# Optimization experiments

Measured on AMD Instinct MI355X. Metric: run time of the kernel, lower is better.

Reference implementation:

```python
import jax, jax.numpy as jnp
import numpy as np

# ---- MACE hyperparameters (match init_kwargs) ----
R_MAX = 5.0      # radial cutoff
P_CUT = 6        # polynomial cutoff exponent
NUM_BESSEL = 8
C = 32           # hidden channels
N_NODES = 50000
N_EDGES = 800000
N_SPECIES = 10
N_GRAPHS = 32
AVG_NEIGH = 16.0
RADIAL_HIDDEN = 64
N_LM = 9                      # (lmax+1)^2, lmax=2
L_OF_LM = np.array([0, 1, 1, 1, 2, 2, 2, 2, 2])


def _sph_harm_l2(v):
    """Real spherical harmonics up to l=2, e3nn 'component' normalization.
    v: [E,3] unit vectors -> [E,9]."""
    x, y, z = v[:, 0], v[:, 1], v[:, 2]
    s3, s5, s15 = 3.0 ** 0.5, 5.0 ** 0.5, 15.0 ** 0.5
    return jnp.stack([
        jnp.ones_like(x),                 # l=0
        s3 * x, s3 * y, s3 * z,           # l=1
        s15 * x * y, s15 * y * z,         # l=2
        (s5 / 2.0) * (3.0 * z * z - 1.0),
        s15 * x * z,
        (s15 / 2.0) * (x * x - y * y),
    ], axis=-1)


def _radial_basis(r):
    """Bessel basis * polynomial cutoff. r: [E] -> [E, NUM_BESSEL]."""
    n = jnp.arange(1, NUM_BESSEL + 1, dtype=r.dtype)
    safe_r = jnp.maximum(r, 1e-9)
    bessel = jnp.sqrt(2.0 / R_MAX) * jnp.sin(n * jnp.pi * safe_r[:, None] / R_MAX) / safe_r[:, None]
    u = r / R_MAX
    p = float(P_CUT)
    fcut = (1.0 - ((p + 1.0) * (p + 2.0) / 2.0) * u ** P_CUT
            + p * (p + 2.0) * u ** (P_CUT + 1)
            - (p * (p + 1.0) / 2.0) * u ** (P_CUT + 2))
    fcut = jnp.where(u < 1.0, fcut, 0.0)
    return bessel * fcut[:, None]


def setup_inputs() -> dict:
    key = jax.random.key(0)
    ks = jax.random.split(key, 12)
    positions = 1.5 * jax.random.normal(ks[0], (N_NODES, 3), dtype=jnp.float32)
    shifts = jnp.zeros((N_EDGES, 3), dtype=jnp.float32)
    species = jax.random.randint(ks[1], (N_NODES,), 0, N_SPECIES)
    node_attrs = jax.nn.one_hot(species, N_SPECIES, dtype=jnp.float32)
    edge_index = jax.random.randint(ks[2], (2, N_EDGES), 0, N_NODES)
    batch = jnp.sort(jax.random.randint(ks[3], (N_NODES,), 0, N_GRAPHS))
    # learned parameters
    W_embed = jax.random.normal(ks[4], (N_SPECIES, C), jnp.float32) / np.sqrt(N_SPECIES)
    rW1 = jax.random.normal(ks[5], (NUM_BESSEL, RADIAL_HIDDEN), jnp.float32) / np.sqrt(NUM_BESSEL)
    rb1 = jnp.zeros((RADIAL_HIDDEN,), jnp.float32)
    rW2 = jax.random.normal(ks[6], (RADIAL_HIDDEN, RADIAL_HIDDEN), jnp.float32) / np.sqrt(RADIAL_HIDDEN)
    rb2 = jnp.zeros((RADIAL_HIDDEN,), jnp.float32)
    rW3 = jax.random.normal(ks[7], (RADIAL_HIDDEN, C * 3), jnp.float32) / np.sqrt(RADIAL_HIDDEN)
    W_mix = jax.random.normal(ks[8], (3, C, C), jnp.float32) / np.sqrt(C)   # per-l channel mixing
    w_quad = jax.random.normal(ks[9], (3,), jnp.float32) * 0.1              # correlation-2 invariant weights
    W_readout = jax.random.normal(ks[10], (C,), jnp.float32) / np.sqrt(C)
    atomic_energies = jax.random.normal(ks[11], (N_SPECIES,), jnp.float32)
    return {"node_attrs": node_attrs, "positions": positions, "shifts": shifts,
            "W_embed": W_embed, "rW1": rW1, "rb1": rb1, "rW2": rW2, "rb2": rb2,
            "rW3": rW3, "W_mix": W_mix, "w_quad": w_quad, "W_readout": W_readout,
            "atomic_energies": atomic_energies, "edge_index": edge_index, "batch": batch}


def reference(node_attrs, positions, shifts, W_embed, rW1, rb1, rW2, rb2, rW3,
              W_mix, w_quad, W_readout, atomic_energies, edge_index, batch):
    sender, receiver = edge_index[0], edge_index[1]
    # edge vectors / lengths (get_edge_vectors_and_lengths)
    vec = positions[receiver] - positions[sender] + shifts          # [E,3]
    length = jnp.linalg.norm(vec, axis=-1)                          # [E]
    unit = vec / jnp.maximum(length, 1e-9)[:, None]
    # radial embedding (Bessel * polynomial cutoff) -> MLP -> per-(channel,l) weights
    rb = _radial_basis(length)                                      # [E,8]
    h1 = jax.nn.silu(rb @ rW1 + rb1)
    h2 = jax.nn.silu(h1 @ rW2 + rb2)
    R = (h2 @ rW3).reshape(-1, C, 3)                                # [E,C,3]
    Y = _sph_harm_l2(unit)                                          # [E,9]
    # node embedding (LinearNodeEmbeddingBlock)
    h = node_attrs @ W_embed                                        # [N,C]
    # channelwise CG tensor product message (scalar source x Y_l -> l) + scatter-sum
    l_of_lm = jnp.asarray(L_OF_LM)
    msg = R[:, :, l_of_lm] * h[sender][:, :, None] * Y[:, None, :]  # [E,C,9]
    A = jax.ops.segment_sum(msg, receiver, num_segments=N_NODES) / AVG_NEIGH  # [N,C,9]
    # per-l linear channel mixing (o3.Linear)
    W_lm = W_mix[l_of_lm]                                           # [9,C,C]
    A2 = jnp.einsum('mcd,ncm->ndm', W_lm, A)                        # [N,C,9]
    # symmetric contraction (correlation 2): rotation-invariant features
    sq = A2 * A2                                                    # [N,C,9]
    onehot_l = jax.nn.one_hot(l_of_lm, 3, dtype=A2.dtype)           # [9,3]
    l_norms = jnp.einsum('ncm,ml->ncl', sq, onehot_l)               # [N,C,3]
    B = A2[:, :, 0] + l_norms @ w_quad                              # [N,C]
    # readout + atomic reference energies, pooled per graph
    node_e = B @ W_readout + node_attrs @ atomic_energies           # [N]
    graph_e = jax.ops.segment_sum(node_e, batch, num_segments=N_GRAPHS)
    return graph_e
```

## Files before the change

### kernel.cpp

```cpp
#include <hip/hip_runtime.h>
#include <hip/hip_bf16.h>

#define NNODES 50000
#define NEDGES 800000
#define NGRAPHS 32
#define NSPEC 10
#define CC 32
#define RH 64
#define NB 8

#define EBLK 128
#define NCHUNK (NEDGES / EBLK)
#define GSTR 136
#define YSTRF 132
#define ASTR 72
#define RBSTR 40
#define SCAN_N 53248

typedef __bf16 bf16x8 __attribute__((ext_vector_type(8)));
typedef float f32x4 __attribute__((ext_vector_type(4)));

__device__ __forceinline__ unsigned pack2bf(float a, float b) {
    return (unsigned)__bfloat16_as_ushort(__float2bfloat16(a)) |
           ((unsigned)__bfloat16_as_ushort(__float2bfloat16(b)) << 16);
}

__global__ __launch_bounds__(256) void prep_hist_kernel(
    const float* __restrict__ attrs, const int* __restrict__ eidx,
    const float* __restrict__ rW1, const float* __restrict__ rb1,
    const float* __restrict__ rW2, const float* __restrict__ rW3,
    int* __restrict__ counts, int* __restrict__ rank, int* __restrict__ species,
    __hip_bfloat16* __restrict__ W1T, __hip_bfloat16* __restrict__ W2T,
    __hip_bfloat16* __restrict__ W3T) {
    int g = blockIdx.x * 256 + threadIdx.x;
    if (g < NEDGES) rank[g] = atomicAdd(&counts[eidx[NEDGES + g]], 1);
    if (g < NNODES) {
        float acc = 0.f;
#pragma unroll
        for (int s = 0; s < NSPEC; ++s) acc += attrs[g * NSPEC + s] * (float)s;
        species[g] = (int)(acc + 0.5f);
    }
    if (g < 64 * 32) {
        int c = g >> 5, k = g & 31;
        float v = (k < 8) ? rW1[k * 64 + c] : ((k == 8) ? rb1[c] : 0.f);
        W1T[g] = __float2bfloat16(v);
    }
    if (g < 64 * 64) {
        int c = g >> 6, k = g & 63;
        W2T[g] = __float2bfloat16(rW2[k * 64 + c]);
    }
    if (g < 96 * 64) {
        int c = g >> 6, k = g & 63;
        W3T[g] = __float2bfloat16(rW3[k * 96 + c]);
    }
}

__global__ __launch_bounds__(1024) void scan_kernel(const int* __restrict__ counts,
                                                    int* __restrict__ offsets) {
    __shared__ int sums[1024];
    const int t = threadIdx.x;
    const int base = t * 52;
    int loc[52];
    int s = 0;
#pragma unroll
    for (int i = 0; i < 13; ++i) {
        int4 v = *(const int4*)&counts[base + i * 4];
        loc[i * 4 + 0] = v.x; loc[i * 4 + 1] = v.y;
        loc[i * 4 + 2] = v.z; loc[i * 4 + 3] = v.w;
        s += v.x + v.y + v.z + v.w;
    }
    sums[t] = s;
    __syncthreads();
    for (int off = 1; off < 1024; off <<= 1) {
        int add = (t >= off) ? sums[t - off] : 0;
        __syncthreads();
        sums[t] += add;
        __syncthreads();
    }
    int run = sums[t] - s;
#pragma unroll
    for (int i = 0; i < 13; ++i) {
        int4 o;
        o.x = run; run += loc[i * 4 + 0];
        o.y = run; run += loc[i * 4 + 1];
        o.z = run; run += loc[i * 4 + 2];
        o.w = run; run += loc[i * 4 + 3];
        *(int4*)&offsets[base + i * 4] = o;
    }
}

__global__ __launch_bounds__(256) void scatter_kernel(const int* __restrict__ eidx,
                                                      const int* __restrict__ offsets,
                                                      const int* __restrict__ rank,
                                                      int* __restrict__ perm) {
    int e = blockIdx.x * 256 + threadIdx.x;
    if (e >= NEDGES) return;
    int rcv = eidx[NEDGES + e];
    perm[offsets[rcv] + rank[e]] = e;
}

__device__ __forceinline__ void flushseg(float* __restrict__ A, int node, int cur,
                                         int nseg, int cbase, int j, float aj, float a8) {
    float* Ap = A + (size_t)node * (CC * 9) + cbase * 9;
    if (cur == 0 || cur == nseg - 1) {
        atomicAdd(Ap + j, aj);
        if (j == 0) atomicAdd(Ap + 8, a8);
    } else {
        Ap[j] = aj;
        if (j == 0) Ap[8] = a8;
    }
}

template <int P>
__device__ __forceinline__ void pass_store_reduce(
    const f32x4 (&acc3)[4][6], const int (&sp_r)[4][4],
    __hip_bfloat16* Gt, const float* Yt, const float* WembLds,
    const unsigned short* rcv_s, const unsigned long long* bal_s,
    float* __restrict__ A, int tid, int w, int lnlo, int q4) {
#pragma unroll
    for (int nti = 0; nti < 3; ++nti) {
        const int nt = P * 3 + nti;
        const int col = nt * 16 + lnlo;
        const int cch = col / 3;
        const int s = nti * 16 + lnlo;
#pragma unroll
        for (int mt = 0; mt < 4; ++mt) {
            const float f0 = acc3[mt][nt][0] * WembLds[sp_r[mt][0] * 32 + cch];
            const float f1 = acc3[mt][nt][1] * WembLds[sp_r[mt][1] * 32 + cch];
            const float f2 = acc3[mt][nt][2] * WembLds[sp_r[mt][2] * 32 + cch];
            const float f3 = acc3[mt][nt][3] * WembLds[sp_r[mt][3] * 32 + cch];
            uint2 pk;
            pk.x = pack2bf(f0, f1);
            pk.y = pack2bf(f2, f3);
            *(uint2*)&Gt[s * GSTR + w * 64 + mt * 16 + q4 * 4] = pk;
        }
    }
    __syncthreads();

    {
        const int c = tid >> 3;
        const int j = tid & 7;
        const int l_j = (j == 0) ? 0 : ((j < 4) ? 1 : 2);
        const uint4* gj = (const uint4*)(Gt + (3 * c + l_j) * GSTR);
        const uint4* g8 = (const uint4*)(Gt + (3 * c + 2) * GSTR);
        const float4* yj = (const float4*)(Yt + j * YSTRF);
        const float4* y8f = (const float4*)(Yt + 8 * YSTRF);
        const unsigned long long b0 = bal_s[0], b1 = bal_s[1];
        const int nseg = __popcll(b0) + __popcll(b1);
        const int cbase = P * 16 + c;

        float aj = 0.f, a8 = 0.f;
        int cur = 0;
        int node = rcv_s[0];

        for (int ch = 0; ch < 16; ++ch) {
            unsigned msk = (unsigned)(((ch < 8) ? (b0 >> (ch * 8)) : (b1 >> ((ch - 8) * 8))) & 0xffull);
            if (ch == 0) msk &= ~1u;
            const uint4 gv = gj[ch];
            const float4 ya = yj[2 * ch];
            const float4 yb = yj[2 * ch + 1];
            uint4 gv8 = {0, 0, 0, 0};
            float4 y8a = {0.f, 0.f, 0.f, 0.f}, y8b = {0.f, 0.f, 0.f, 0.f};
            if (j == 0) { gv8 = g8[ch]; y8a = y8f[2 * ch]; y8b = y8f[2 * ch + 1]; }
            const unsigned gw[4] = {gv.x, gv.y, gv.z, gv.w};
            const unsigned gw8[4] = {gv8.x, gv8.y, gv8.z, gv8.w};
            const float yf[8] = {ya.x, ya.y, ya.z, ya.w, yb.x, yb.y, yb.z, yb.w};
            const float yf8[8] = {y8a.x, y8a.y, y8a.z, y8a.w, y8b.x, y8b.y, y8b.z, y8b.w};
#pragma unroll
            for (int i = 0; i < 8; ++i) {
                if (msk & (1u << i)) {
                    flushseg(A, node, cur, nseg, cbase, j, aj, a8);
                    aj = 0.f; a8 = 0.f; ++cur;
                    node = rcv_s[ch * 8 + i];
                }
                const unsigned gu = gw[i >> 1];
                const float gf = __uint_as_float((i & 1) ? (gu & 0xffff0000u) : (gu << 16));
                aj = fmaf(gf, yf[i], aj);
                if (j == 0) {
                    const unsigned hu = gw8[i >> 1];
                    const float hf = __uint_as_float((i & 1) ? (hu & 0xffff0000u) : (hu << 16));
                    a8 = fmaf(hf, yf8[i], a8);
                }
            }
        }
        flushseg(A, node, cur, nseg, cbase, j, aj, a8);
    }
    __syncthreads();
}

__global__ __launch_bounds__(EBLK, 3) void edge_kernel(
    const float* __restrict__ pos, const float* __restrict__ shifts,
    const int* __restrict__ eidx, const int* __restrict__ perm,
    const __hip_bfloat16* __restrict__ W1T, const __hip_bfloat16* __restrict__ W2T,
    const __hip_bfloat16* __restrict__ W3T, const float* __restrict__ rb2,
    const int* __restrict__ species, const float* __restrict__ Wemb,
    float* __restrict__ A) {
    __shared__ __align__(16) short smem_u[128 * ASTR];
    __shared__ __align__(16) float Yt[9 * YSTRF];
    __shared__ float WembLds[NSPEC * CC];
    __shared__ float rb2L[RH];
    __shared__ unsigned short rcv_s[EBLK];
    __shared__ unsigned char spec_s[EBLK];
    __shared__ unsigned long long bal_s[2];

    __hip_bfloat16* act = (__hip_bfloat16*)smem_u;
    __hip_bfloat16* Gt = (__hip_bfloat16*)smem_u;
    __hip_bfloat16* rbA = (__hip_bfloat16*)smem_u;

    const int tid = threadIdx.x;
    const int lane = tid & 63;
    const int w = tid >> 6;
    const int lnlo = lane & 15;
    const int q4 = lane >> 4;

    const int slot = blockIdx.x * EBLK + tid;
    const int eid = perm[slot];
    const int snd = eidx[eid];
    const int rcv = eidx[NEDGES + eid];

    const float vx = pos[rcv * 3 + 0] - pos[snd * 3 + 0] + shifts[eid * 3 + 0];
    const float vy = pos[rcv * 3 + 1] - pos[snd * 3 + 1] + shifts[eid * 3 + 1];
    const float vz = pos[rcv * 3 + 2] - pos[snd * 3 + 2] + shifts[eid * 3 + 2];
    const float r = sqrtf(vx * vx + vy * vy + vz * vz);
    const float safe_r = fmaxf(r, 1e-9f);
    const float rinv = 1.f / safe_r;
    const float ux = vx * rinv, uy = vy * rinv, uz = vz * rinv;

    {
        const float s3 = 1.7320508075688772f;
        const float s15 = 3.872983346207417f;
        const float s15h = 1.9364916731037085f;
        const float s5h = 1.118033988749895f;
        Yt[0 * YSTRF + tid] = 1.f;
        Yt[1 * YSTRF + tid] = s3 * ux;
        Yt[2 * YSTRF + tid] = s3 * uy;
        Yt[3 * YSTRF + tid] = s3 * uz;
        Yt[4 * YSTRF + tid] = s15 * ux * uy;
        Yt[5 * YSTRF + tid] = s15 * uy * uz;
        Yt[6 * YSTRF + tid] = s5h * (3.f * uz * uz - 1.f);
        Yt[7 * YSTRF + tid] = s15 * ux * uz;
        Yt[8 * YSTRF + tid] = s15h * (ux * ux - uy * uy);
        rcv_s[tid] = (unsigned short)rcv;
        spec_s[tid] = (unsigned char)species[snd];
        for (int i = tid; i < NSPEC * CC; i += EBLK) WembLds[i] = Wemb[i];
        if (tid < RH) rb2L[tid] = rb2[tid];
    }

    {
        const float u = r * 0.2f;
        const float u2 = u * u;
        const float u6 = u2 * u2 * u2;
        const float u7 = u6 * u;
        const float u8v = u7 * u;
        float fcut = 1.f - 28.f * u6 + 48.f * u7 - 21.f * u8v;
        fcut = (u < 1.f) ? fcut : 0.f;
        const float pref = 0.632455532f * rinv * fcut;
        float rb[NB];
#pragma unroll
        for (int k = 0; k < NB; ++k) {
            const float fk = (float)(k + 1) * 0.628318530718f;
            rb[k] = __sinf(fk * safe_r) * pref;
        }
        uint4 v0, v1;
        v0.x = pack2bf(rb[0], rb[1]); v0.y = pack2bf(rb[2], rb[3]);
        v0.z = pack2bf(rb[4], rb[5]); v0.w = pack2bf(rb[6], rb[7]);
        v1.x = 0x3F80u; v1.y = 0u; v1.z = 0u; v1.w = 0u;
        uint4 vz4 = {0u, 0u, 0u, 0u};
        *(uint4*)&rbA[tid * RBSTR + 0] = v0;
        *(uint4*)&rbA[tid * RBSTR + 8] = v1;
        *(uint4*)&rbA[tid * RBSTR + 16] = vz4;
        *(uint4*)&rbA[tid * RBSTR + 24] = vz4;
    }

    __syncthreads();
    {
        const bool head = (tid == 0) || (rcv_s[tid] != rcv_s[tid - 1]);
        const unsigned long long bal = __ballot(head);
        if ((tid & 63) == 0) bal_s[tid >> 6] = bal;
    }

    f32x4 acc1[4][4];
#pragma unroll
    for (int mt = 0; mt < 4; ++mt)
#pragma unroll
        for (int nt = 0; nt < 4; ++nt) acc1[mt][nt] = (f32x4){0.f, 0.f, 0.f, 0.f};
    {
        bf16x8 a1[4], b1[4];
#pragma unroll
        for (int mt = 0; mt < 4; ++mt)
            a1[mt] = *(const bf16x8*)&rbA[(w * 64 + mt * 16 + lnlo) * RBSTR + q4 * 8];
#pragma unroll
        for (int nt = 0; nt < 4; ++nt)
            b1[nt] = *(const bf16x8*)&W1T[(nt * 16 + lnlo) * 32 + q4 * 8];
        __syncthreads();
#pragma unroll
        for (int mt = 0; mt < 4; ++mt)
#pragma unroll
            for (int nt = 0; nt < 4; ++nt)
                acc1[mt][nt] = __builtin_amdgcn_mfma_f32_16x16x32_bf16(
                    a1[mt], b1[nt], acc1[mt][nt], 0, 0, 0);
    }

#pragma unroll
    for (int mt = 0; mt < 4; ++mt)
#pragma unroll
        for (int nt = 0; nt < 4; ++nt)
#pragma unroll
            for (int rr = 0; rr < 4; ++rr) {
                const float x = acc1[mt][nt][rr];
                act[(w * 64 + mt * 16 + q4 * 4 + rr) * ASTR + nt * 16 + lnlo] =
                    __float2bfloat16(x / (1.f + __expf(-x)));
            }
    __syncthreads();

    f32x4 acc2[4][4];
#pragma unroll
    for (int mt = 0; mt < 4; ++mt)
#pragma unroll
        for (int nt = 0; nt < 4; ++nt) acc2[mt][nt] = (f32x4){0.f, 0.f, 0.f, 0.f};
    {
        bf16x8 a2[4][2], b2[4][2];
#pragma unroll
        for (int mt = 0; mt < 4; ++mt)
#pragma unroll
            for (int kk = 0; kk < 2; ++kk)
                a2[mt][kk] = *(const bf16x8*)&act[(w * 64 + mt * 16 + lnlo) * ASTR + kk * 32 + q4 * 8];
#pragma unroll
        for (int nt = 0; nt < 4; ++nt)
#pragma unroll
            for (int kk = 0; kk < 2; ++kk)
                b2[nt][kk] = *(const bf16x8*)&W2T[(nt * 16 + lnlo) * 64 + kk * 32 + q4 * 8];
#pragma unroll
        for (int kk = 0; kk < 2; ++kk)
#pragma unroll
            for (int mt = 0; mt < 4; ++mt)
#pragma unroll
                for (int nt = 0; nt < 4; ++nt)
                    acc2[mt][nt] = __builtin_amdgcn_mfma_f32_16x16x32_bf16(
                        a2[mt][kk], b2[nt][kk], acc2[mt][nt], 0, 0, 0);
    }
    __syncthreads();

#pragma unroll
    for (int mt = 0; mt < 4; ++mt)
#pragma unroll
        for (int nt = 0; nt < 4; ++nt) {
            const float bias = rb2L[nt * 16 + lnlo];
#pragma unroll
            for (int rr = 0; rr < 4; ++rr) {
                const float x = acc2[mt][nt][rr] + bias;
                act[(w * 64 + mt * 16 + q4 * 4 + rr) * ASTR + nt * 16 + lnlo] =
                    __float2bfloat16(x / (1.f + __expf(-x)));
            }
        }
    __syncthreads();

    f32x4 acc3[4][6];
#pragma unroll
    for (int mt = 0; mt < 4; ++mt)
#pragma unroll
        for (int nt = 0; nt < 6; ++nt) acc3[mt][nt] = (f32x4){0.f, 0.f, 0.f, 0.f};
    {
        bf16x8 a3[4][2], b3[6][2];
#pragma unroll
        for (int mt = 0; mt < 4; ++mt)
#pragma unroll
            for (int kk = 0; kk < 2; ++kk)
                a3[mt][kk] = *(const bf16x8*)&act[(w * 64 + mt * 16 + lnlo) * ASTR + kk * 32 + q4 * 8];
#pragma unroll
        for (int nt = 0; nt < 6; ++nt)
#pragma unroll
            for (int kk = 0; kk < 2; ++kk)
                b3[nt][kk] = *(const bf16x8*)&W3T[(nt * 16 + lnlo) * 64 + kk * 32 + q4 * 8];
#pragma unroll
        for (int kk = 0; kk < 2; ++kk)
#pragma unroll
            for (int mt = 0; mt < 4; ++mt)
#pragma unroll
                for (int nt = 0; nt < 6; ++nt)
                    acc3[mt][nt] = __builtin_amdgcn_mfma_f32_16x16x32_bf16(
                        a3[mt][kk], b3[nt][kk], acc3[mt][nt], 0, 0, 0);
    }
    __syncthreads();

    int sp_r[4][4];
#pragma unroll
    for (int mt = 0; mt < 4; ++mt)
#pragma unroll
        for (int rr = 0; rr < 4; ++rr)
            sp_r[mt][rr] = (int)spec_s[w * 64 + mt * 16 + q4 * 4 + rr];

    pass_store_reduce<0>(acc3, sp_r, Gt, Yt, WembLds, rcv_s, bal_s, A, tid, w, lnlo, q4);
    pass_store_reduce<1>(acc3, sp_r, Gt, Yt, WembLds, rcv_s, bal_s, A, tid, w, lnlo, q4);
}

__global__ __launch_bounds__(256) void node_kernel(
    const float* __restrict__ A, const float* __restrict__ Wmix,
    const float* __restrict__ wquad, const float* __restrict__ Wread,
    const float* __restrict__ attrs, const float* __restrict__ ae,
    const int* __restrict__ batch, float* __restrict__ out) {
    __shared__ float Ald[8][CC * 9];
    __shared__ float ne_s[8];
    __shared__ int g_s[8];
    const int t = threadIdx.x;
    const int ln = t >> 5;
    const int d = t & 31;
    const int n = blockIdx.x * 8 + ln;

    const float* Arow = A + (size_t)n * (CC * 9);
#pragma unroll
    for (int i = 0; i < 9; ++i) Ald[ln][d + 32 * i] = Arow[d + 32 * i] * (1.f / 16.f);
    __syncthreads();

    float A2[9];
#pragma unroll
    for (int m = 0; m < 9; ++m) {
        const int l = (m == 0) ? 0 : ((m < 4) ? 1 : 2);
        float acc = 0.f;
#pragma unroll
        for (int cch = 0; cch < CC; ++cch)
            acc = fmaf(Wmix[(l * CC + cch) * CC + d], Ald[ln][cch * 9 + m], acc);
        A2[m] = acc;
    }

    const float q0 = wquad[0], q1 = wquad[1], q2 = wquad[2];
    const float n0 = A2[0] * A2[0];
    const float n1 = A2[1] * A2[1] + A2[2] * A2[2] + A2[3] * A2[3];
    const float n2 = A2[4] * A2[4] + A2[5] * A2[5] + A2[6] * A2[6] + A2[7] * A2[7] + A2[8] * A2[8];
    const float B = A2[0] + n0 * q0 + n1 * q1 + n2 * q2;

    float v = B * Wread[d];
#pragma unroll
    for (int off = 16; off; off >>= 1) v += __shfl_xor(v, off, 32);

    if (d == 0) {
        float ne = v;
#pragma unroll
        for (int s = 0; s < NSPEC; ++s) ne += attrs[n * NSPEC + s] * ae[s];
        ne_s[ln] = ne;
        g_s[ln] = batch[n];
    }
    __syncthreads();
    if (t == 0) {
        float acc = ne_s[0];
        int g = g_s[0];
#pragma unroll
        for (int i = 1; i < 8; ++i) {
            if (g_s[i] == g) acc += ne_s[i];
            else { atomicAdd(&out[g], acc); g = g_s[i]; acc = ne_s[i]; }
        }
        atomicAdd(&out[g], acc);
    }
}

extern "C" void kernel_launch(void* const* d_in, const int* in_sizes, int n_in,
                              void* d_out, int out_size, void* d_ws, size_t ws_size,
                              hipStream_t stream) {
    const float* attrs  = (const float*)d_in[0];
    const float* pos    = (const float*)d_in[1];
    const float* shifts = (const float*)d_in[2];
    const float* Wemb   = (const float*)d_in[3];
    const float* rW1    = (const float*)d_in[4];
    const float* rb1    = (const float*)d_in[5];
    const float* rW2    = (const float*)d_in[6];
    const float* rb2    = (const float*)d_in[7];
    const float* rW3    = (const float*)d_in[8];
    const float* Wmix   = (const float*)d_in[9];
    const float* wquad  = (const float*)d_in[10];
    const float* Wread  = (const float*)d_in[11];
    const float* ae     = (const float*)d_in[12];
    const int* eidx     = (const int*)d_in[13];
    const int* batch    = (const int*)d_in[14];
    float* out = (float*)d_out;

    char* wsp = (char*)d_ws;
    float* A      = (float*)wsp;  wsp += (size_t)NNODES * CC * 9 * 4;
    int* rank     = (int*)A;
    int* perm     = (int*)wsp;    wsp += (size_t)NEDGES * 4;
    int* offsets  = (int*)wsp;    wsp += (size_t)SCAN_N * 4;
    int* counts   = (int*)wsp;    wsp += (size_t)SCAN_N * 4;
    int* species  = (int*)wsp;    wsp += (size_t)NNODES * 4;
    __hip_bfloat16* W1T = (__hip_bfloat16*)wsp; wsp += 64 * 32 * 2;
    __hip_bfloat16* W2T = (__hip_bfloat16*)wsp; wsp += 64 * 64 * 2;
    __hip_bfloat16* W3T = (__hip_bfloat16*)wsp; wsp += 96 * 64 * 2;

    hipMemsetAsync(counts, 0, (size_t)SCAN_N * sizeof(int), stream);
    hipMemsetAsync(out, 0, NGRAPHS * sizeof(float), stream);

    prep_hist_kernel<<<NEDGES / 256, 256, 0, stream>>>(attrs, eidx, rW1, rb1, rW2, rW3,
                                                       counts, rank, species, W1T, W2T, W3T);
    scan_kernel<<<1, 1024, 0, stream>>>(counts, offsets);
    scatter_kernel<<<NEDGES / 256, 256, 0, stream>>>(eidx, offsets, rank, perm);

    hipMemsetAsync(A, 0, (size_t)NNODES * CC * 9 * sizeof(float), stream);

    edge_kernel<<<NCHUNK, EBLK, 0, stream>>>(pos, shifts, eidx, perm,
                                             W1T, W2T, W3T, rb2, species, Wemb, A);
    node_kernel<<<NNODES / 8, 256, 0, stream>>>(A, Wmix, wquad, Wread, attrs, ae, batch, out);
}
```

Baseline: 321.1 us.

## Replace full A memset with boundary-only zeroing and transpose radial MLP MFMAs

Drops the full memset of the node accumulator A. A small kernel now zeroes only the rows of receivers at chunk boundaries, which are the only rows that get atomic adds. Interior segments are written directly, and node_kernel masks nodes with zero in-degree using counts, so stale workspace data is ignored. The radial MLP MFMAs are also transposed so that silu outputs can be stored as packed 8-byte writes. The l=2 m=8 reduction moves to lane j=7 to reuse its own G row, and species extraction reads attrs through shared memory with coalesced loads. This relies on every row being fully written or zeroed. Interior writes overlap the A buffer that also holds rank, which is safe only because of the launch ordering.

```diff
diff --git a/kernel.cpp b/kernel.cpp
--- a/kernel.cpp
+++ b/kernel.cpp
@@ -24,6 +24,7 @@
     return (unsigned)__bfloat16_as_ushort(__float2bfloat16(a)) |
            ((unsigned)__bfloat16_as_ushort(__float2bfloat16(b)) << 16);
 }
+__device__ __forceinline__ float silu(float x) { return x / (1.f + __expf(-x)); }
 
 __global__ __launch_bounds__(256) void prep_hist_kernel(
     const float* __restrict__ attrs, const int* __restrict__ eidx,
@@ -32,13 +33,23 @@
     int* __restrict__ counts, int* __restrict__ rank, int* __restrict__ species,
     __hip_bfloat16* __restrict__ W1T, __hip_bfloat16* __restrict__ W2T,
     __hip_bfloat16* __restrict__ W3T) {
-    int g = blockIdx.x * 256 + threadIdx.x;
+    __shared__ float at[256 * NSPEC];
+    const int tid = threadIdx.x;
+    int g = blockIdx.x * 256 + tid;
     if (g < NEDGES) rank[g] = atomicAdd(&counts[eidx[NEDGES + g]], 1);
-    if (g < NNODES) {
-        float acc = 0.f;
-#pragma unroll
-        for (int s = 0; s < NSPEC; ++s) acc += attrs[g * NSPEC + s] * (float)s;
-        species[g] = (int)(acc + 0.5f);
+    const int nbase = blockIdx.x * 256;
+    if (nbase < NNODES) {
+        for (int i = tid; i < 256 * NSPEC; i += 256) {
+            int idx = nbase * NSPEC + i;
+            at[i] = (idx < NNODES * NSPEC) ? attrs[idx] : 0.f;
+        }
+        __syncthreads();
+        if (g < NNODES) {
+            float acc = 0.f;
+#pragma unroll
+            for (int s = 0; s < NSPEC; ++s) acc += at[tid * NSPEC + s] * (float)s;
+            species[g] = (int)(acc + 0.5f);
+        }
     }
     if (g < 64 * 32) {
         int c = g >> 5, k = g & 31;
@@ -99,15 +110,27 @@
     perm[offsets[rcv] + rank[e]] = e;
 }
 
+__global__ __launch_bounds__(576) void zero_bounds_kernel(const int* __restrict__ perm,
+                                                          const int* __restrict__ eidx,
+                                                          float* __restrict__ A) {
+    const int c = blockIdx.x;
+    const int t = threadIdx.x;
+    const int slot = (t < 288) ? c * EBLK : (c * EBLK + EBLK - 1);
+    const int e = perm[slot];
+    const int rcv = eidx[NEDGES + e];
+    A[(size_t)rcv * (CC * 9) + (t % 288)] = 0.f;
+}
+
 __device__ __forceinline__ void flushseg(float* __restrict__ A, int node, int cur,
-                                         int nseg, int cbase, int j, float aj, float a8) {
+                                         int nseg, int cbase, int j, bool wr8,
+                                         float aj, float a8) {
     float* Ap = A + (size_t)node * (CC * 9) + cbase * 9;
     if (cur == 0 || cur == nseg - 1) {
         atomicAdd(Ap + j, aj);
-        if (j == 0) atomicAdd(Ap + 8, a8);
+        if (wr8) atomicAdd(Ap + 8, a8);
     } else {
         Ap[j] = aj;
-        if (j == 0) Ap[8] = a8;
+        if (wr8) Ap[8] = a8;
     }
 }
 
@@ -140,9 +163,9 @@
     {
         const int c = tid >> 3;
         const int j = tid & 7;
+        const bool m8 = (j == 7);
         const int l_j = (j == 0) ? 0 : ((j < 4) ? 1 : 2);
         const uint4* gj = (const uint4*)(Gt + (3 * c + l_j) * GSTR);
-        const uint4* g8 = (const uint4*)(Gt + (3 * c + 2) * GSTR);
         const float4* yj = (const float4*)(Yt + j * YSTRF);
         const float4* y8f = (const float4*)(Yt + 8 * YSTRF);
         const unsigned long long b0 = bal_s[0], b1 = bal_s[1];
@@ -159,31 +182,25 @@
             const uint4 gv = gj[ch];
             const float4 ya = yj[2 * ch];
             const float4 yb = yj[2 * ch + 1];
-            uint4 gv8 = {0, 0, 0, 0};
             float4 y8a = {0.f, 0.f, 0.f, 0.f}, y8b = {0.f, 0.f, 0.f, 0.f};
-            if (j == 0) { gv8 = g8[ch]; y8a = y8f[2 * ch]; y8b = y8f[2 * ch + 1]; }
+            if (m8) { y8a = y8f[2 * ch]; y8b = y8f[2 * ch + 1]; }
             const unsigned gw[4] = {gv.x, gv.y, gv.z, gv.w};
-            const unsigned gw8[4] = {gv8.x, gv8.y, gv8.z, gv8.w};
             const float yf[8] = {ya.x, ya.y, ya.z, ya.w, yb.x, yb.y, yb.z, yb.w};
             const float yf8[8] = {y8a.x, y8a.y, y8a.z, y8a.w, y8b.x, y8b.y, y8b.z, y8b.w};
 #pragma unroll
             for (int i = 0; i < 8; ++i) {
                 if (msk & (1u << i)) {
-                    flushseg(A, node, cur, nseg, cbase, j, aj, a8);
+                    flushseg(A, node, cur, nseg, cbase, j, m8, aj, a8);
                     aj = 0.f; a8 = 0.f; ++cur;
                     node = rcv_s[ch * 8 + i];
                 }
                 const unsigned gu = gw[i >> 1];
                 const float gf = __uint_as_float((i & 1) ? (gu & 0xffff0000u) : (gu << 16));
                 aj = fmaf(gf, yf[i], aj);
-                if (j == 0) {
-                    const unsigned hu = gw8[i >> 1];
-                    const float hf = __uint_as_float((i & 1) ? (hu & 0xffff0000u) : (hu << 16));
-                    a8 = fmaf(hf, yf8[i], a8);
-                }
+                if (m8) a8 = fmaf(gf, yf8[i], a8);
             }
         }
-        flushseg(A, node, cur, nseg, cbase, j, aj, a8);
+        flushseg(A, node, cur, nseg, cbase, j, m8, aj, a8);
     }
     __syncthreads();
 }
@@ -281,78 +298,81 @@
 
     f32x4 acc1[4][4];
 #pragma unroll
-    for (int mt = 0; mt < 4; ++mt)
-#pragma unroll
-        for (int nt = 0; nt < 4; ++nt) acc1[mt][nt] = (f32x4){0.f, 0.f, 0.f, 0.f};
-    {
-        bf16x8 a1[4], b1[4];
-#pragma unroll
-        for (int mt = 0; mt < 4; ++mt)
-            a1[mt] = *(const bf16x8*)&rbA[(w * 64 + mt * 16 + lnlo) * RBSTR + q4 * 8];
-#pragma unroll
-        for (int nt = 0; nt < 4; ++nt)
-            b1[nt] = *(const bf16x8*)&W1T[(nt * 16 + lnlo) * 32 + q4 * 8];
+    for (int jt = 0; jt < 4; ++jt)
+#pragma unroll
+        for (int et = 0; et < 4; ++et) acc1[jt][et] = (f32x4){0.f, 0.f, 0.f, 0.f};
+    {
+        bf16x8 wf[4], af[4];
+#pragma unroll
+        for (int jt = 0; jt < 4; ++jt)
+            wf[jt] = *(const bf16x8*)&W1T[(jt * 16 + lnlo) * 32 + q4 * 8];
+#pragma unroll
+        for (int et = 0; et < 4; ++et)
+            af[et] = *(const bf16x8*)&rbA[(w * 64 + et * 16 + lnlo) * RBSTR + q4 * 8];
         __syncthreads();
 #pragma unroll
-        for (int mt = 0; mt < 4; ++mt)
-#pragma unroll
-            for (int nt = 0; nt < 4; ++nt)
-                acc1[mt][nt] = __builtin_amdgcn_mfma_f32_16x16x32_bf16(
-                    a1[mt], b1[nt], acc1[mt][nt], 0, 0, 0);
-    }
-
-#pragma unroll
-    for (int mt = 0; mt < 4; ++mt)
-#pragma unroll
-        for (int nt = 0; nt < 4; ++nt)
-#pragma unroll
-            for (int rr = 0; rr < 4; ++rr) {
-                const float x = acc1[mt][nt][rr];
-                act[(w * 64 + mt * 16 + q4 * 4 + rr) * ASTR + nt * 16 + lnlo] =
-                    __float2bfloat16(x / (1.f + __expf(-x)));
-            }
+        for (int jt = 0; jt < 4; ++jt)
+#pragma unroll
+            for (int et = 0; et < 4; ++et)
+                acc1[jt][et] = __builtin_amdgcn_mfma_f32_16x16x32_bf16(
+                    wf[jt], af[et], acc1[jt][et], 0, 0, 0);
+    }
+
+#pragma unroll
+    for (int jt = 0; jt < 4; ++jt) {
+        const int ch0 = jt * 16 + q4 * 4;
+#pragma unroll
+        for (int et = 0; et < 4; ++et) {
+            const int e = w * 64 + et * 16 + lnlo;
+            uint2 pk;
+            pk.x = pack2bf(silu(acc1[jt][et][0]), silu(acc1[jt][et][1]));
+            pk.y = pack2bf(silu(acc1[jt][et][2]), silu(acc1[jt][et][3]));
+            *(uint2*)&act[e * ASTR + ch0] = pk;
+        }
+    }
     __syncthreads();
 
     f32x4 acc2[4][4];
 #pragma unroll
-    for (int mt = 0; mt < 4; ++mt)
-#pragma unroll
-        for (int nt = 0; nt < 4; ++nt) acc2[mt][nt] = (f32x4){0.f, 0.f, 0.f, 0.f};
-    {
-        bf16x8 a2[4][2], b2[4][2];
-#pragma unroll
-        for (int mt = 0; mt < 4; ++mt)
+    for (int jt = 0; jt < 4; ++jt)
+#pragma unroll
+        for (int et = 0; et < 4; ++et) acc2[jt][et] = (f32x4){0.f, 0.f, 0.f, 0.f};
+    {
+        bf16x8 wf[4][2], af[4][2];
+#pragma unroll
+        for (int jt = 0; jt < 4; ++jt)
 #pragma unroll
             for (int kk = 0; kk < 2; ++kk)
-                a2[mt][kk] = *(const bf16x8*)&act[(w * 64 + mt * 16 + lnlo) * ASTR + kk * 32 + q4 * 8];
-#pragma unroll
-        for (int nt = 0; nt < 4; ++nt)
+                wf[jt][kk] = *(const bf16x8*)&W2T[(jt * 16 + lnlo) * 64 + kk * 32 + q4 * 8];
+#pragma unroll
+        for (int et = 0; et < 4; ++et)
 #pragma unroll
             for (int kk = 0; kk < 2; ++kk)
-                b2[nt][kk] = *(const bf16x8*)&W2T[(nt * 16 + lnlo) * 64 + kk * 32 + q4 * 8];
+                af[et][kk] = *(const bf16x8*)&act[(w * 64 + et * 16 + lnlo) * ASTR + kk * 32 + q4 * 8];
 #pragma unroll
         for (int kk = 0; kk < 2; ++kk)
 #pragma unroll
-            for (int mt = 0; mt < 4; ++mt)
-#pragma unroll
-                for (int nt = 0; nt < 4; ++nt)
-                    acc2[mt][nt] = __builtin_amdgcn_mfma_f32_16x16x32_bf16(
-                        a2[mt][kk], b2[nt][kk], acc2[mt][nt], 0, 0, 0);
-    }
-    __syncthreads();
-
-#pragma unroll
-    for (int mt = 0; mt < 4; ++mt)
-#pragma unroll
-        for (int nt = 0; nt < 4; ++nt) {
-            const float bias = rb2L[nt * 16 + lnlo];
-#pragma unroll
-            for (int rr = 0; rr < 4; ++rr) {
-                const float x = acc2[mt][nt][rr] + bias;
-                act[(w * 64 + mt * 16 + q4 * 4 + rr) * ASTR + nt * 16 + lnlo] =
-                    __float2bfloat16(x / (1.f + __expf(-x)));
-            }
-        }
+            for (int jt = 0; jt < 4; ++jt)
+#pragma unroll
+                for (int et = 0; et < 4; ++et)
+                    acc2[jt][et] = __builtin_amdgcn_mfma_f32_16x16x32_bf16(
+                        wf[jt][kk], af[et][kk], acc2[jt][et], 0, 0, 0);
+    }
+    __syncthreads();
+
+#pragma unroll
+    for (int jt = 0; jt < 4; ++jt) {
+        const int ch0 = jt * 16 + q4 * 4;
+        const float4 bv = *(const float4*)&rb2L[ch0];
+#pragma unroll
+        for (int et = 0; et < 4; ++et) {
+            const int e = w * 64 + et * 16 + lnlo;
+            uint2 pk;
+            pk.x = pack2bf(silu(acc2[jt][et][0] + bv.x), silu(acc2[jt][et][1] + bv.y));
+            pk.y = pack2bf(silu(acc2[jt][et][2] + bv.z), silu(acc2[jt][et][3] + bv.w));
+            *(uint2*)&act[e * ASTR + ch0] = pk;
+        }
+    }
     __syncthreads();
 
     f32x4 acc3[4][6];
@@ -398,7 +418,8 @@
     const float* __restrict__ A, const float* __restrict__ Wmix,
     const float* __restrict__ wquad, const float* __restrict__ Wread,
     const float* __restrict__ attrs, const float* __restrict__ ae,
-    const int* __restrict__ batch, float* __restrict__ out) {
+    const int* __restrict__ batch, const int* __restrict__ counts,
+    float* __restrict__ out) {
     __shared__ float Ald[8][CC * 9];
     __shared__ float ne_s[8];
     __shared__ int g_s[8];
@@ -407,9 +428,10 @@
     const int d = t & 31;
     const int n = blockIdx.x * 8 + ln;
 
+    const float sc = (counts[n] != 0) ? (1.f / 16.f) : 0.f;
     const float* Arow = A + (size_t)n * (CC * 9);
 #pragma unroll
-    for (int i = 0; i < 9; ++i) Ald[ln][d + 32 * i] = Arow[d + 32 * i] * (1.f / 16.f);
+    for (int i = 0; i < 9; ++i) Ald[ln][d + 32 * i] = Arow[d + 32 * i] * sc;
     __syncthreads();
 
     float A2[9];
@@ -491,10 +513,10 @@
                                                        counts, rank, species, W1T, W2T, W3T);
     scan_kernel<<<1, 1024, 0, stream>>>(counts, offsets);
     scatter_kernel<<<NEDGES / 256, 256, 0, stream>>>(eidx, offsets, rank, perm);
-
-    hipMemsetAsync(A, 0, (size_t)NNODES * CC * 9 * sizeof(float), stream);
+    zero_bounds_kernel<<<NCHUNK, 576, 0, stream>>>(perm, eidx, A);
 
     edge_kernel<<<NCHUNK, EBLK, 0, stream>>>(pos, shifts, eidx, perm,
                                              W1T, W2T, W3T, rb2, species, Wemb, A);
-    node_kernel<<<NNODES / 8, 256, 0, stream>>>(A, Wmix, wquad, Wread, attrs, ae, batch, out);
-}
+    node_kernel<<<NNODES / 8, 256, 0, stream>>>(A, Wmix, wquad, Wread, attrs, ae, batch,
+                                                counts, out);
+}
```

Measured after the change: 309.5 us. -3.6%, faster.
